# Performance work log

Hardware: AMD Instinct MI355X
Metric: run time of the kernel (lower is better)

## Reference

```python
import jax, jax.numpy as jnp
import numpy as np

B_SZ, SEQ = 2, 4096
D_MODEL, D_STATE, D_CONV, HEADDIM = 768, 128, 4, 64
D_INNER = 1536
NHEADS = D_INNER // HEADDIM  # 24
D_XBC = D_INNER + 2 * D_STATE  # 1792
D_PROJ = 2 * D_INNER + 2 * D_STATE + NHEADS  # 3352
CHUNK = 128
EPS = 1e-5


def setup_inputs():
    key = jax.random.key(0)
    ks = jax.random.split(key, 10)
    feature = jax.random.normal(ks[0], (B_SZ, SEQ, D_MODEL), jnp.float32)
    in_proj_w = jax.random.normal(ks[1], (D_PROJ, D_MODEL), jnp.float32) * 0.02
    conv_w = jax.random.normal(ks[2], (D_XBC, D_CONV), jnp.float32) * 0.2
    conv_b = jax.random.normal(ks[3], (D_XBC,), jnp.float32) * 0.02
    dt_bias = jnp.log(jnp.expm1(jax.random.uniform(ks[4], (NHEADS,), jnp.float32, 0.001, 0.1)))
    A_log = jnp.log(jax.random.uniform(ks[5], (NHEADS,), jnp.float32, 1.0, 16.0))
    D = jax.random.normal(ks[6], (NHEADS,), jnp.float32) * 0.1 + 1.0
    norm_w = jnp.ones((D_INNER,), jnp.float32)
    out_proj_w = jax.random.normal(ks[7], (D_MODEL, D_INNER), jnp.float32) * 0.02
    gate1 = jnp.float32(0.6)
    return {"feature": feature, "gate1": gate1, "in_proj_w": in_proj_w, "conv_w": conv_w,
            "conv_b": conv_b, "dt_bias": dt_bias, "A_log": A_log, "D": D,
            "norm_w": norm_w, "out_proj_w": out_proj_w}


def segsum(x):
    # x: (..., T) -> (..., T, T); out[..., i, j] = sum_{k=j+1..i} x[..., k]; -inf above diagonal
    T = x.shape[-1]
    xc = jnp.cumsum(x, axis=-1)
    d = xc[..., :, None] - xc[..., None, :]
    mask = jnp.tril(jnp.ones((T, T), bool))
    return jnp.where(mask, d, -jnp.inf)


def ssd(xd, Adt, B, C):
    # Chunked SSD (Mamba2 selective scan). xd: (b,L,H,P) = x*dt; Adt: (b,L,H); B,C: (b,L,N)
    b, L, H, P = xd.shape
    c, Q = L // CHUNK, CHUNK
    xd = xd.reshape(b, c, Q, H, P)
    Adt = Adt.reshape(b, c, Q, H).transpose(0, 3, 1, 2)          # (b,H,c,Q)
    Bc = B.reshape(b, c, Q, -1)
    Cc = C.reshape(b, c, Q, -1)
    A_cum = jnp.cumsum(Adt, axis=-1)                             # (b,H,c,Q)
    Lmat = jnp.exp(segsum(Adt))                                  # (b,H,c,Q,Q)
    CB = jnp.einsum('bcln,bcsn->bcls', Cc, Bc)                   # (b,c,Q,Q)
    Y_diag = jnp.einsum('bcls,bhcls,bcshp->bclhp', CB, Lmat, xd)
    decay_states = jnp.exp(A_cum[..., -1:] - A_cum)              # (b,H,c,Q)
    states = jnp.einsum('bcln,bhcl,bclhp->bchpn', Bc, decay_states, xd)  # (b,c,H,P,N)
    A_last = A_cum[..., -1]                                      # (b,H,c)
    decay_chunk = jnp.exp(segsum(jnp.pad(A_last, ((0, 0), (0, 0), (1, 0)))))  # (b,H,c+1,c+1)
    states_pad = jnp.concatenate([jnp.zeros_like(states[:, :1]), states], axis=1)
    prev = jnp.einsum('bhzc,bchpn->bzhpn', decay_chunk, states_pad)[:, :-1]   # state at chunk start
    Y_off = jnp.einsum('bcln,bhcl,bchpn->bclhp', Cc, jnp.exp(A_cum), prev)
    return (Y_diag + Y_off).reshape(b, L, H, P)


def reference(feature, gate1, in_proj_w, conv_w, conv_b, dt_bias, A_log, D, norm_w, out_proj_w):
    b, L, _ = feature.shape
    zxbcdt = feature @ in_proj_w.T                               # (b,L,3352)
    z = zxbcdt[..., :D_INNER]
    xBC = zxbcdt[..., D_INNER:D_INNER + D_XBC]
    dt = jax.nn.softplus(zxbcdt[..., -NHEADS:] + dt_bias)       # (b,L,H)
    # causal depthwise conv1d (kernel=4) + SiLU
    xp = jnp.pad(xBC, ((0, 0), (D_CONV - 1, 0), (0, 0)))
    xconv = sum(conv_w[:, k] * xp[:, k:k + L, :] for k in range(D_CONV)) + conv_b
    xBC = jax.nn.silu(xconv)
    x = xBC[..., :D_INNER].reshape(b, L, NHEADS, HEADDIM)
    Bm = xBC[..., D_INNER:D_INNER + D_STATE]
    Cm = xBC[..., D_INNER + D_STATE:]
    A = -jnp.exp(A_log)                                          # (H,)
    y = ssd(x * dt[..., None], dt * A, Bm, Cm) + D[:, None] * x  # skip term D*x
    y = y.reshape(b, L, D_INNER)
    # gated RMSNorm (norm_before_gate=False): gate first, then rmsnorm
    y = y * jax.nn.silu(z)
    y = y * jax.lax.rsqrt(jnp.mean(y * y, axis=-1, keepdims=True) + EPS) * norm_w
    out = y @ out_proj_w.T                                       # out_proj (bias=False)
    return jax.nn.sigmoid(gate1) * out + feature
```

## Files before the change

### kernel.cpp

```cpp
#include <hip/hip_runtime.h>
#include <hip/hip_bf16.h>
#include <math.h>

#define B_SZ 2
#define SEQ 4096
#define DMODEL 768
#define DSTATE 128
#define HEADDIM 64
#define DINNER 1536
#define NHEADS 24
#define DXBC 1792
#define DPROJ 3352
#define NPAD1 3456
#define CHUNK 128
#define NCHUNK 32
#define ROWS (B_SZ*SEQ)
#define LDTC 136
#define LDTT 132
#define LDE 136
#define LDE2 132
#define LDEY 65

typedef float floatx4 __attribute__((ext_vector_type(4)));
typedef __bf16 bf16x8 __attribute__((ext_vector_type(8)));

__device__ __forceinline__ float sigmoidf_(float x){ return 1.f/(1.f+__expf(-x)); }
__device__ __forceinline__ float siluf_(float x){ return x/(1.f+__expf(-x)); }
__device__ __forceinline__ float softplusf_(float x){ return (x>20.f)? x : __logf(1.f+__expf(x)); }
__device__ __forceinline__ __bf16 cvt_bf(float x){ __hip_bfloat16 t = __float2bfloat16(x); return *(__bf16*)&t; }

__device__ __forceinline__ void gload_lds16(const __hip_bfloat16* g, __hip_bfloat16* l){
    __builtin_amdgcn_global_load_lds(
        (const __attribute__((address_space(1))) void*)g,
        (__attribute__((address_space(3))) void*)l, 16, 0, 0);
}

__global__ __launch_bounds__(512)
void gemm1_mfma(const __hip_bfloat16* __restrict__ A,
                const __hip_bfloat16* __restrict__ W,
                __hip_bfloat16* __restrict__ z16, __hip_bfloat16* __restrict__ xbc16,
                float* __restrict__ dtb, const float* __restrict__ dt_bias)
{
    __shared__ __align__(16) char smem[49152];
    __hip_bfloat16* Asm = (__hip_bfloat16*)smem;
    __hip_bfloat16* Wsm = Asm + 256*64;
    const int tid = threadIdx.x;
    const int lane = tid & 63, wave = tid >> 6;
    const int blk = blockIdx.x;
    const int m_tile = ((blk & 7) << 2) | ((blk >> 3) & 3);
    const int bx = blk >> 5;
    const int bm = m_tile*256, bn = bx*128;
    const int wm = (wave & 3)*64, wn = (wave >> 2)*64;
    const int r16 = lane & 15, qbase = lane >> 4, sw = r16 & 7;
    floatx4 acc[4][4] = {};
    for (int k0 = 0; k0 < DMODEL; k0 += 64) {
#pragma unroll
        for (int j = 0; j < 4; ++j) {
            int cc = j*512 + tid;
            int row = cc >> 3, jc = cc & 7;
            int sj = jc ^ (row & 7);
            gload_lds16(A + (size_t)(bm+row)*DMODEL + k0 + sj*8, Asm + cc*8);
        }
#pragma unroll
        for (int j = 0; j < 2; ++j) {
            int cc = j*512 + tid;
            int row = cc >> 3, jc = cc & 7;
            int sj = jc ^ (row & 7);
            gload_lds16(W + (size_t)(bn+row)*DMODEL + k0 + sj*8, Wsm + cc*8);
        }
        __syncthreads();
#pragma unroll
        for (int ks = 0; ks < 2; ++ks) {
            const int kq = ((qbase + ks*4) ^ sw)*8;
            bf16x8 af[4], wf[4];
#pragma unroll
            for (int i = 0; i < 4; ++i) {
                af[i] = *(const bf16x8*)(Asm + (wm + i*16 + r16)*64 + kq);
                wf[i] = *(const bf16x8*)(Wsm + (wn + i*16 + r16)*64 + kq);
            }
#pragma unroll
            for (int mi = 0; mi < 4; ++mi)
#pragma unroll
                for (int ni = 0; ni < 4; ++ni)
                    acc[mi][ni] = __builtin_amdgcn_mfma_f32_16x16x32_bf16(
                        af[mi], wf[ni], acc[mi][ni], 0, 0, 0);
        }
        __syncthreads();
    }
    const int col = lane & 15, rowq = (lane >> 4)*4;
    if (bx == 26) {
        if (wn == 0) {
#pragma unroll
            for (int mi = 0; mi < 4; ++mi)
#pragma unroll
                for (int ni = 0; ni < 2; ++ni) {
                    int h = ni*16 + col;
                    if (h < NHEADS)
#pragma unroll
                        for (int r = 0; r < 4; ++r) {
                            int m = bm + wm + mi*16 + rowq + r;
                            dtb[(size_t)m*NHEADS + h] =
                                softplusf_(acc[mi][ni][r] + dt_bias[h]);
                        }
                }
        }
        return;
    }
    __hip_bfloat16* Tsm = (__hip_bfloat16*)smem;
    __hip_bfloat16* dst; int ldd;
    if (bx < 12) { dst = z16 + bn;            ldd = DINNER; }
    else         { dst = xbc16 + bn - DINNER; ldd = DXBC;  }
    for (int half = 0; half < 2; ++half) {
        if (((wave & 3) >> 1) == half) {
#pragma unroll
            for (int mi = 0; mi < 4; ++mi)
#pragma unroll
                for (int ni = 0; ni < 4; ++ni)
#pragma unroll
                    for (int r = 0; r < 4; ++r)
                        Tsm[(wm - half*128 + mi*16 + rowq + r)*LDE + wn + ni*16 + col] =
                            __float2bfloat16(acc[mi][ni][r]);
        }
        __syncthreads();
#pragma unroll
        for (int it = 0; it < 4; ++it) {
            int e = it*512 + tid;
            int row = e >> 4, c0 = (e & 15)*8;
            bf16x8 v = *(const bf16x8*)(Tsm + row*LDE + c0);
            *(bf16x8*)(dst + (size_t)(bm + half*128 + row)*ldd + c0) = v;
        }
        __syncthreads();
    }
}

__global__ __launch_bounds__(256)
void gemm2_mfma(const __hip_bfloat16* __restrict__ A,
                const __hip_bfloat16* __restrict__ W,
                float* __restrict__ C,
                const float* __restrict__ gate, const float* __restrict__ resid,
                const float* __restrict__ rowsq)
{
    __shared__ __align__(16) char smem[33792];
    __shared__ float scale_lds[128];
    __hip_bfloat16* Asm = (__hip_bfloat16*)smem;
    __hip_bfloat16* Wsm = Asm + 128*64;
    const int tid = threadIdx.x;
    const int lane = tid & 63, wave = tid >> 6;
    const int blk = blockIdx.x;
    const int mblk = blk & 63;
    const int m_tile = ((mblk & 7) << 3) | (mblk >> 3);
    const int bm = m_tile*128, bn = (blk >> 6)*128;
    const int wm = (wave & 1)*64, wn = (wave >> 1)*64;
    const int r16 = lane & 15, qbase = lane >> 4, sw = r16 & 7;
    floatx4 acc[4][4] = {};
    for (int k0 = 0; k0 < DINNER; k0 += 64) {
#pragma unroll
        for (int j = 0; j < 4; ++j) {
            int cc = j*256 + tid;
            int row = cc >> 3, jc = cc & 7;
            int sj = jc ^ (row & 7);
            gload_lds16(A + (size_t)(bm+row)*DINNER + k0 + sj*8, Asm + cc*8);
        }
#pragma unroll
        for (int j = 0; j < 4; ++j) {
            int cc = j*256 + tid;
            int row = cc >> 3, jc = cc & 7;
            int sj = jc ^ (row & 7);
            gload_lds16(W + (size_t)(bn+row)*DINNER + k0 + sj*8, Wsm + cc*8);
        }
        __syncthreads();
#pragma unroll
        for (int ks = 0; ks < 2; ++ks) {
            const int kq = ((qbase + ks*4) ^ sw)*8;
            bf16x8 af[4], wf[4];
#pragma unroll
            for (int i = 0; i < 4; ++i) {
                af[i] = *(const bf16x8*)(Asm + (wm + i*16 + r16)*64 + kq);
                wf[i] = *(const bf16x8*)(Wsm + (wn + i*16 + r16)*64 + kq);
            }
#pragma unroll
            for (int mi = 0; mi < 4; ++mi)
#pragma unroll
                for (int ni = 0; ni < 4; ++ni)
                    acc[mi][ni] = __builtin_amdgcn_mfma_f32_16x16x32_bf16(
                        af[mi], wf[ni], acc[mi][ni], 0, 0, 0);
        }
        __syncthreads();
    }
    if (tid < 128)
        scale_lds[tid] = rsqrtf(rowsq[bm + tid] * (1.f/DINNER) + 1e-5f);
    float gs = sigmoidf_(gate[0]);
    __syncthreads();
    const int col = lane & 15, rowq = (lane >> 4)*4;
    float* Tsm = (float*)smem;
    for (int half = 0; half < 2; ++half) {
        if ((wave & 1) == half) {
#pragma unroll
            for (int mi = 0; mi < 4; ++mi)
#pragma unroll
                for (int ni = 0; ni < 4; ++ni)
#pragma unroll
                    for (int r = 0; r < 4; ++r)
                        Tsm[(mi*16 + rowq + r)*LDE2 + wn + ni*16 + col] = acc[mi][ni][r];
        }
        __syncthreads();
#pragma unroll
        for (int it = 0; it < 8; ++it) {
            int e = it*256 + tid;
            int row = e >> 5, c0 = (e & 31)*4;
            float4 v = *(const float4*)(Tsm + row*LDE2 + c0);
            float sc = gs * scale_lds[half*64 + row];
            size_t off = (size_t)(bm + half*64 + row)*DMODEL + bn + c0;
            float4 rv = *(const float4*)(resid + off);
            v.x = sc*v.x + rv.x; v.y = sc*v.y + rv.y;
            v.z = sc*v.z + rv.z; v.w = sc*v.w + rv.w;
            *(float4*)(C + off) = v;
        }
        __syncthreads();
    }
}

#define NC1 (ROWS*DMODEL)
#define NC2 (NPAD1*DMODEL)
#define NC3 (DMODEL*DINNER)
#define NV1 (NC1/8)
#define NV2 (NC2/8)
#define NV3 (NC3/8)
#define NVR (ROWS/8)
__global__ __launch_bounds__(256)
void cast_all(const float* __restrict__ feature, const float* __restrict__ in_w,
              const float* __restrict__ out_w, const float* __restrict__ nw,
              __hip_bfloat16* __restrict__ fbf, __hip_bfloat16* __restrict__ wbf,
              __hip_bfloat16* __restrict__ owbf, float* __restrict__ rowsq)
{
    int v = blockIdx.x*256 + threadIdx.x;
    if (v < NV1) {
        int i = v*8;
        float4 a = *(const float4*)(feature + i);
        float4 b = *(const float4*)(feature + i + 4);
        bf16x8 o;
        o[0]=cvt_bf(a.x); o[1]=cvt_bf(a.y); o[2]=cvt_bf(a.z); o[3]=cvt_bf(a.w);
        o[4]=cvt_bf(b.x); o[5]=cvt_bf(b.y); o[6]=cvt_bf(b.z); o[7]=cvt_bf(b.w);
        *(bf16x8*)(fbf + i) = o;
    } else if (v < NV1 + NV2) {
        int j = (v - NV1)*8;
        int n = j / DMODEL, k = j - n*DMODEL;
        bf16x8 o;
        if (n < DPROJ) {
            const float* s = in_w + (size_t)n*DMODEL + k;
            float4 a = *(const float4*)(s);
            float4 b = *(const float4*)(s + 4);
            o[0]=cvt_bf(a.x); o[1]=cvt_bf(a.y); o[2]=cvt_bf(a.z); o[3]=cvt_bf(a.w);
            o[4]=cvt_bf(b.x); o[5]=cvt_bf(b.y); o[6]=cvt_bf(b.z); o[7]=cvt_bf(b.w);
        } else {
#pragma unroll
            for (int q = 0; q < 8; ++q) o[q] = (__bf16)0.f;
        }
        *(bf16x8*)(wbf + j) = o;
    } else if (v < NV1 + NV2 + NV3) {
        int j = (v - NV1 - NV2)*8;
        int k = j % DINNER;
        float4 a  = *(const float4*)(out_w + j);
        float4 b  = *(const float4*)(out_w + j + 4);
        float4 na = *(const float4*)(nw + k);
        float4 nb = *(const float4*)(nw + k + 4);
        bf16x8 o;
        o[0]=cvt_bf(a.x*na.x); o[1]=cvt_bf(a.y*na.y); o[2]=cvt_bf(a.z*na.z); o[3]=cvt_bf(a.w*na.w);
        o[4]=cvt_bf(b.x*nb.x); o[5]=cvt_bf(b.y*nb.y); o[6]=cvt_bf(b.z*nb.z); o[7]=cvt_bf(b.w*nb.w);
        *(bf16x8*)(owbf + j) = o;
    } else if (v < NV1 + NV2 + NV3 + NVR) {
        int j = (v - NV1 - NV2 - NV3)*8;
        float4 z = {0.f, 0.f, 0.f, 0.f};
        *(float4*)(rowsq + j) = z;
        *(float4*)(rowsq + j + 4) = z;
    }
}

__global__ __launch_bounds__(512)
void conv_scan_k(const __hip_bfloat16* __restrict__ xbc16, const float* __restrict__ cw,
                 const float* __restrict__ cbias,
                 __hip_bfloat16* __restrict__ x_t,
                 __hip_bfloat16* __restrict__ B_n, __hip_bfloat16* __restrict__ B_t,
                 __hip_bfloat16* __restrict__ C_n,
                 const float* __restrict__ dtb, const float* __restrict__ A_log,
                 float* __restrict__ acum)
{
    int xb = blockIdx.x;
    int tid = threadIdx.x;
    if (xb >= 14) {
        __shared__ float wtot;
        int h = xb - 14, c = blockIdx.y, b = blockIdx.z;
        int lane = tid & 63;
        float s = 0.f;
        if (tid < 128) {
            float Aa = -__expf(A_log[h]);
            s = dtb[((size_t)b*SEQ + c*CHUNK + tid)*NHEADS + h] * Aa;
#pragma unroll
            for (int off = 1; off < 64; off <<= 1) {
                float t = __shfl_up(s, off);
                if (lane >= off) s += t;
            }
            if (tid == 63) wtot = s;
        }
        __syncthreads();
        if (tid >= 64 && tid < 128) s += wtot;
        if (tid < 128)
            acum[((b*NHEADS+h)*NCHUNK + c)*CHUNK + tid] = s;
        return;
    }
    __shared__ __align__(16) __hip_bfloat16 in[131*LDTC];
    __shared__ __align__(16) __hip_bfloat16 T[128*LDTT];
    int ct = xb, lt = blockIdx.y, b = blockIdx.z;
    int base = lt*128;
    for (int it = 0; it < 2096; it += 512) {
        int e = it + tid; if (e >= 2096) break;
        int row = e >> 4, c0 = (e & 15)*8;
        int l = base - 3 + row;
        bf16x8 v;
        if (l < 0) { for (int j = 0; j < 8; ++j) v[j] = (__bf16)0.f; }
        else v = *(const bf16x8*)(xbc16 + ((size_t)b*SEQ + l)*DXBC + ct*128 + c0);
        *(bf16x8*)(in + row*LDTC + c0) = v;
    }
    __syncthreads();
    int ch = tid & 127, lh = tid >> 7, l0 = lh*32;
    int g = ct*128 + ch;
    float w0 = cw[g*4+0], w1 = cw[g*4+1], w2 = cw[g*4+2], w3 = cw[g*4+3];
    float bias = cbias[g];
    float a0 = __bfloat162float(in[(l0+0)*LDTC + ch]);
    float a1 = __bfloat162float(in[(l0+1)*LDTC + ch]);
    float a2 = __bfloat162float(in[(l0+2)*LDTC + ch]);
#pragma unroll
    for (int li = 0; li < 32; ++li) {
        float a3 = __bfloat162float(in[(l0+li+3)*LDTC + ch]);
        float o = siluf_(bias + w0*a0 + w1*a1 + w2*a2 + w3*a3);
        a0 = a1; a1 = a2; a2 = a3;
        __hip_bfloat16 ob = __float2bfloat16(o);
        size_t rr = (size_t)b*SEQ + base + l0 + li;
        if (ct == 12)      B_n[rr*DSTATE + ch] = ob;
        else if (ct == 13) C_n[rr*DSTATE + ch] = ob;
        if (ct <= 12)
            T[ch*LDTT + l0 + li] = ob;
    }
    if (ct <= 12) {
        __syncthreads();
        __hip_bfloat16* dst = (ct < 12) ? x_t : B_t;
#pragma unroll
        for (int it = 0; it < 4; ++it) {
            int e = it*512 + tid;
            int chn = e >> 4, c0 = (e & 15)*8;
            int g2 = ct*128 + chn;
            size_t trow = (ct < 12)
                ? ((size_t)b*NHEADS + (g2>>6))*HEADDIM + (g2 & 63)
                : (size_t)b*DSTATE + chn;
            bf16x8 v = *(const bf16x8*)(T + chn*LDTT + c0);
            *(bf16x8*)(dst + trow*SEQ + base + c0) = v;
        }
    }
}

__global__ __launch_bounds__(256)
void cbst_k(const __hip_bfloat16* __restrict__ B_n, const __hip_bfloat16* __restrict__ C_n,
            __hip_bfloat16* __restrict__ CB16,
            const __hip_bfloat16* __restrict__ x_t, const __hip_bfloat16* __restrict__ B_t,
            const float* __restrict__ dtb, const float* __restrict__ acum,
            __hip_bfloat16* __restrict__ states)
{
    __shared__ __align__(16) __hip_bfloat16 BT[128*128];
    __shared__ float f[128];
    int bid = blockIdx.x;
    int tid = threadIdx.x, lane = tid & 63, wave = tid >> 6;
    if (bid < 64) {
        int c = bid & 31, b = bid >> 5;
        size_t base = (size_t)b*SEQ + c*CHUNK;
        int r16 = lane & 15, kq = (lane>>4)*8;
        floatx4 acc[2][8] = {};
#pragma unroll
        for (int ks = 0; ks < 4; ++ks) {
            int k0 = ks*32 + kq;
            bf16x8 af[2], bfv[8];
#pragma unroll
            for (int mt = 0; mt < 2; ++mt)
                af[mt] = *(const bf16x8*)(C_n + (base + (wave*2+mt)*16 + r16)*DSTATE + k0);
#pragma unroll
            for (int st = 0; st < 8; ++st)
                bfv[st] = *(const bf16x8*)(B_n + (base + st*16 + r16)*DSTATE + k0);
#pragma unroll
            for (int mt = 0; mt < 2; ++mt)
#pragma unroll
                for (int st = 0; st < 8; ++st)
                    if (st <= wave*2+mt)
                        acc[mt][st] = __builtin_amdgcn_mfma_f32_16x16x32_bf16(
                            af[mt], bfv[st], acc[mt][st], 0,0,0);
        }
        size_t cbb = (size_t)(b*NCHUNK+c)*CHUNK*CHUNK;
        int scol = lane & 15, rowq = (lane>>4)*4;
#pragma unroll
        for (int mt = 0; mt < 2; ++mt)
#pragma unroll
            for (int st = 0; st < 8; ++st)
                if (st <= wave*2+mt)
#pragma unroll
                    for (int r = 0; r < 4; ++r)
                        CB16[cbb + (size_t)((wave*2+mt)*16 + rowq + r)*CHUNK + st*16 + scol] =
                            __float2bfloat16(acc[mt][st][r]);
        return;
    }
    int t = bid - 64;
    int c = t & 31;
    int h = (t>>5) % NHEADS;
    int b = t/(32*NHEADS);
    int arow = ((b*NHEADS+h)*NCHUNK + c)*CHUNK;
    size_t rbase = (size_t)b*SEQ + c*CHUNK;
    int cl = c*CHUNK;
#pragma unroll
    for (int j = 0; j < 8; ++j) {
        int cc = j*256 + tid;
        int n = cc >> 4, chk = cc & 15;
        int sj = chk ^ (n & 7);
        gload_lds16(B_t + ((size_t)b*DSTATE + n)*SEQ + cl + sj*8, BT + cc*8);
    }
    if (tid < 128) {
        float alast = acum[arow + 127];
        f[tid] = dtb[(rbase + tid)*NHEADS + h] * __expf(alast - acum[arow + tid]);
    }
    __syncthreads();
    int r16 = lane & 15, kq = (lane>>4)*8;
    size_t xtb = ((size_t)b*NHEADS + h)*HEADDIM;
    floatx4 acc[8] = {};
#pragma unroll
    for (int ks = 0; ks < 4; ++ks) {
        int k0 = ks*32 + kq;
        bf16x8 xa = *(const bf16x8*)(x_t + (xtb + wave*16 + r16)*SEQ + cl + k0);
        bf16x8 af;
#pragma unroll
        for (int j = 0; j < 8; ++j)
            af[j] = (__bf16)((float)xa[j] * f[k0 + j]);
        int chL = k0 >> 3;
        bf16x8 bfv[8];
#pragma unroll
        for (int nt = 0; nt < 8; ++nt) {
            int row = nt*16 + r16;
            bfv[nt] = *(const bf16x8*)(BT + (row*16 + (chL ^ (row & 7)))*8);
        }
#pragma unroll
        for (int nt = 0; nt < 8; ++nt)
            acc[nt] = __builtin_amdgcn_mfma_f32_16x16x32_bf16(af, bfv[nt], acc[nt], 0,0,0);
    }
    size_t sb = ((size_t)(b*NCHUNK+c)*NHEADS + h)*(HEADDIM*DSTATE);
    int ncol = lane & 15, rowq = (lane>>4)*4;
#pragma unroll
    for (int nt = 0; nt < 8; ++nt)
#pragma unroll
        for (int r = 0; r < 4; ++r)
            states[sb + (size_t)(wave*16 + rowq + r)*DSTATE + nt*16 + ncol] =
                __float2bfloat16(acc[nt][r]);
}

__global__ __launch_bounds__(64)
void recur_k(__hip_bfloat16* __restrict__ states, const float* __restrict__ acum)
{
    int pb = blockIdx.x & 15;
    int bh = blockIdx.x >> 4;
    int h = bh % NHEADS, b = bh / NHEADS;
    int voff = (pb*64 + threadIdx.x)*8;
    const size_t cstride = (size_t)NHEADS*HEADDIM*DSTATE;
    size_t base0 = ((size_t)(b*NCHUNK)*NHEADS + h)*(HEADDIM*DSTATE) + voff;
    bf16x8 st[NCHUNK];
    float ev[NCHUNK];
#pragma unroll
    for (int c = 0; c < NCHUNK; ++c)
        st[c] = *(const bf16x8*)(states + base0 + (size_t)c*cstride);
#pragma unroll
    for (int c = 0; c < NCHUNK; ++c)
        ev[c] = __expf(acum[((b*NHEADS+h)*NCHUNK + c)*CHUNK + 127]);
    float S[8] = {};
#pragma unroll
    for (int c = 0; c < NCHUNK; ++c) {
        bf16x8 pv;
#pragma unroll
        for (int j = 0; j < 8; ++j) {
            pv[j] = (__bf16)S[j];
            S[j] = S[j]*ev[c] + (float)st[c][j];
        }
        *(bf16x8*)(states + base0 + (size_t)c*cstride) = pv;
    }
}

__global__ __launch_bounds__(512, 4)
void y_mfma(const __hip_bfloat16* __restrict__ x_t, const __hip_bfloat16* __restrict__ z16,
            const __hip_bfloat16* __restrict__ C_n, const __hip_bfloat16* __restrict__ CB16,
            const __hip_bfloat16* __restrict__ states, const float* __restrict__ dtb,
            const float* __restrict__ acum, const float* __restrict__ Dp,
            __hip_bfloat16* __restrict__ y16, float* __restrict__ rowsq)
{
    __shared__ __align__(16) char smem[32768];
    __hip_bfloat16* XT = (__hip_bfloat16*)smem;
    __hip_bfloat16* ST = XT + 64*128;
    __shared__ __align__(16) float Tsm[128*LDEY];
    __shared__ float ac[128], dts[128], gk[128];
    const int tid = threadIdx.x, lane = tid & 63, wave = tid >> 6;
    const int r16 = lane & 15, kq = (lane>>4)*8;
    const int l = wave*16 + r16;
    const int pcol = lane & 15, rowq = (lane>>4)*4;
    const int erow = tid >> 2, ec0 = (tid & 3)*16;
    const int NU = B_SZ*NHEADS*NCHUNK;
    {
        int u = blockIdx.x;
        int c = u & 31, h = (u>>5) % NHEADS, b = u/(32*NHEADS);
        size_t xtb = ((size_t)b*NHEADS + h)*HEADDIM;
        size_t sb  = ((size_t)(b*NCHUNK+c)*NHEADS + h)*(HEADDIM*DSTATE);
        int cl = c*CHUNK;
#pragma unroll
        for (int j = 0; j < 2; ++j) {
            int cc = j*512 + tid;
            int p = cc >> 4, ch = cc & 15;
            int sj = ch ^ (p & 7);
            gload_lds16(x_t + (xtb + p)*SEQ + cl + sj*8, XT + cc*8);
            gload_lds16(states + sb + (size_t)p*DSTATE + sj*8, ST + cc*8);
        }
    }
#pragma unroll 1
    for (int u = blockIdx.x; u < NU; u += 512) {
        int c = u & 31;
        int h = (u>>5) % NHEADS;
        int b = u/(32*NHEADS);
        int arow = ((b*NHEADS+h)*NCHUNK + c)*CHUNK;
        size_t rbase = (size_t)b*SEQ + c*CHUNK;
        size_t cbb = (size_t)(b*NCHUNK+c)*CHUNK*CHUNK;
        if (tid < 128) {
            ac[tid]  = acum[arow + tid];
            dts[tid] = dtb[(rbase + tid)*NHEADS + h];
        }
        __syncthreads();
        if (tid < 128)
            gk[tid] = __expf(ac[tid & 96] - ac[tid]) * dts[tid];
        bf16x8 cb[4], cv[4];
#pragma unroll
        for (int ks = 0; ks < 4; ++ks) {
            cb[ks] = *(const bf16x8*)(CB16 + cbb + (size_t)l*CHUNK + ks*32 + kq);
            cv[ks] = *(const bf16x8*)(C_n + (rbase + l)*DSTATE + ks*32 + kq);
        }
        bf16x8 zA = *(const bf16x8*)(z16 + (rbase + erow)*DINNER + h*HEADDIM + ec0);
        bf16x8 zB = *(const bf16x8*)(z16 + (rbase + erow)*DINNER + h*HEADDIM + ec0 + 8);
        __syncthreads();
        float acl = ac[l];
        float Dh = Dp[h];
        floatx4 acc[4] = {};
        int nks = (wave >> 1) + 1;
#pragma unroll
        for (int ks = 0; ks < 4; ++ks) {
            if (ks < nks) {
                int k0 = ks*32 + kq;
                float fl = __expf(acl - ac[ks*32]);
                bf16x8 af;
#pragma unroll
                for (int j = 0; j < 8; ++j) {
                    int s = k0 + j;
                    float w = (s <= l) ? (float)cb[ks][j] * (fl * gk[s]) : 0.f;
                    if (s == l) w += Dh;
                    af[j] = (__bf16)w;
                }
                int chL = k0 >> 3;
                bf16x8 bfv[4];
#pragma unroll
                for (int pt = 0; pt < 4; ++pt) {
                    int row = pt*16 + r16;
                    bfv[pt] = *(const bf16x8*)(XT + (row*16 + (chL ^ (row & 7)))*8);
                }
#pragma unroll
                for (int pt = 0; pt < 4; ++pt)
                    acc[pt] = __builtin_amdgcn_mfma_f32_16x16x32_bf16(af, bfv[pt], acc[pt], 0,0,0);
            }
        }
        float eal = __expf(acl);
#pragma unroll
        for (int ks = 0; ks < 4; ++ks) {
            int k0 = ks*32 + kq;
            bf16x8 af;
#pragma unroll
            for (int j = 0; j < 8; ++j)
                af[j] = (__bf16)((float)cv[ks][j] * eal);
            int chL = k0 >> 3;
            bf16x8 bfv[4];
#pragma unroll
            for (int pt = 0; pt < 4; ++pt) {
                int row = pt*16 + r16;
                bfv[pt] = *(const bf16x8*)(ST + (row*16 + (chL ^ (row & 7)))*8);
            }
#pragma unroll
            for (int pt = 0; pt < 4; ++pt)
                acc[pt] = __builtin_amdgcn_mfma_f32_16x16x32_bf16(af, bfv[pt], acc[pt], 0,0,0);
        }
        __syncthreads();
        int un = u + 512;
        if (un < NU) {
            int c2 = un & 31, h2 = (un>>5) % NHEADS, b2 = un/(32*NHEADS);
            size_t xtb2 = ((size_t)b2*NHEADS + h2)*HEADDIM;
            size_t sb2  = ((size_t)(b2*NCHUNK+c2)*NHEADS + h2)*(HEADDIM*DSTATE);
            int cl2 = c2*CHUNK;
#pragma unroll
            for (int j = 0; j < 2; ++j) {
                int cc = j*512 + tid;
                int p = cc >> 4, ch = cc & 15;
                int sj = ch ^ (p & 7);
                gload_lds16(x_t + (xtb2 + p)*SEQ + cl2 + sj*8, XT + cc*8);
                gload_lds16(states + sb2 + (size_t)p*DSTATE + sj*8, ST + cc*8);
            }
        }
#pragma unroll
        for (int pt = 0; pt < 4; ++pt)
#pragma unroll
            for (int r = 0; r < 4; ++r)
                Tsm[(wave*16 + rowq + r)*LDEY + pt*16 + pcol] = acc[pt][r];
        __syncthreads();
        {
            float s = 0.f; bf16x8 o1, o2;
#pragma unroll
            for (int j2 = 0; j2 < 8; ++j2) {
                float g = Tsm[erow*LDEY + ec0 + j2] * siluf_(__bfloat162float(zA[j2]));
                o1[j2] = cvt_bf(g); s += g*g;
            }
#pragma unroll
            for (int j2 = 0; j2 < 8; ++j2) {
                float g = Tsm[erow*LDEY + ec0 + 8 + j2] * siluf_(__bfloat162float(zB[j2]));
                o2[j2] = cvt_bf(g); s += g*g;
            }
            size_t grow = rbase + erow;
            *(bf16x8*)(y16 + grow*DINNER + h*HEADDIM + ec0)     = o1;
            *(bf16x8*)(y16 + grow*DINNER + h*HEADDIM + ec0 + 8) = o2;
            s += __shfl_xor(s, 1); s += __shfl_xor(s, 2);
            if ((tid & 3) == 0)
                atomicAdd(rowsq + grow, s);
        }
    }
}

extern "C" void kernel_launch(void* const* d_in, const int* in_sizes, int n_in,
                              void* d_out, int out_size, void* d_ws, size_t ws_size,
                              hipStream_t stream)
{
    const float* feature = (const float*)d_in[0];
    const float* gate1   = (const float*)d_in[1];
    const float* in_w    = (const float*)d_in[2];
    const float* conv_w  = (const float*)d_in[3];
    const float* conv_b  = (const float*)d_in[4];
    const float* dt_bias = (const float*)d_in[5];
    const float* A_log   = (const float*)d_in[6];
    const float* Dp      = (const float*)d_in[7];
    const float* norm_w  = (const float*)d_in[8];
    const float* out_w   = (const float*)d_in[9];
    float* out = (float*)d_out;

    char* p = (char*)d_ws;
    __hip_bfloat16* z16   = (__hip_bfloat16*)p; p += (size_t)ROWS*DINNER*2;
    __hip_bfloat16* xbc16 = (__hip_bfloat16*)p; p += (size_t)ROWS*DXBC*2;
    __hip_bfloat16* x_t   = (__hip_bfloat16*)p; p += (size_t)ROWS*DINNER*2;
    __hip_bfloat16* B_n   = (__hip_bfloat16*)p; p += (size_t)ROWS*DSTATE*2;
    __hip_bfloat16* B_t   = (__hip_bfloat16*)p; p += (size_t)ROWS*DSTATE*2;
    __hip_bfloat16* C_n   = (__hip_bfloat16*)p; p += (size_t)ROWS*DSTATE*2;
    float* dtb    = (float*)p;            p += (size_t)ROWS*NHEADS*4;
    float* acum   = (float*)p;            p += (size_t)B_SZ*NHEADS*NCHUNK*CHUNK*4;
    float* rowsq  = (float*)p;            p += (size_t)ROWS*4;
    __hip_bfloat16* CB16 = (__hip_bfloat16*)p; p += (size_t)B_SZ*NCHUNK*CHUNK*CHUNK*2;
    __hip_bfloat16* states = (__hip_bfloat16*)p; p += (size_t)B_SZ*NCHUNK*NHEADS*HEADDIM*DSTATE*2;
    __hip_bfloat16* y16  = (__hip_bfloat16*)p; p += (size_t)ROWS*DINNER*2;
    __hip_bfloat16* fbf  = (__hip_bfloat16*)p; p += (size_t)ROWS*DMODEL*2;
    __hip_bfloat16* wbf  = (__hip_bfloat16*)p; p += (size_t)NPAD1*DMODEL*2;
    __hip_bfloat16* owbf = (__hip_bfloat16*)p; p += (size_t)DMODEL*DINNER*2;

    cast_all<<<(NV1+NV2+NV3+NVR+255)/256, 256, 0, stream>>>(feature, in_w, out_w, norm_w,
                                                            fbf, wbf, owbf, rowsq);

    gemm1_mfma<<<27*32, 512, 0, stream>>>(fbf, wbf, z16, xbc16, dtb, dt_bias);
    conv_scan_k<<<dim3(14 + NHEADS, 32, B_SZ), 512, 0, stream>>>(
        xbc16, conv_w, conv_b, x_t, B_n, B_t, C_n, dtb, A_log, acum);
    cbst_k<<<64 + B_SZ*NHEADS*NCHUNK, 256, 0, stream>>>(
        B_n, C_n, CB16, x_t, B_t, dtb, acum, states);
    recur_k<<<B_SZ*NHEADS*16, 64, 0, stream>>>(states, acum);
    y_mfma<<<512, 512, 0, stream>>>(x_t, z16, C_n, CB16, states,
                                    dtb, acum, Dp, y16, rowsq);
    gemm2_mfma<<<6*64, 256, 0, stream>>>(y16, owbf, out, gate1, feature, rowsq);
}
```

Baseline: 264.1 us.

## Double-buffer gemm2 LDS, pack scan heads per block, stage B in LDS for CB

The out-projection GEMM now double-buffers its A and W tiles in LDS, issuing the next tile's loads before computing the current one, with one barrier per k-step instead of two. This is meant to hide global load latency, at the cost of doubling LDS to 64KB, which may reduce occupancy. The cumsum blocks in conv_scan now handle four heads each with all 512 threads active, so far fewer mostly-idle blocks are launched. In cbst_k, the CB blocks load the B chunk once into swizzled LDS rather than re-reading it from global memory in every wave.

```diff
diff --git a/kernel.cpp b/kernel.cpp
--- a/kernel.cpp
+++ b/kernel.cpp
@@ -140,10 +140,12 @@
                 const float* __restrict__ gate, const float* __restrict__ resid,
                 const float* __restrict__ rowsq)
 {
-    __shared__ __align__(16) char smem[33792];
+    __shared__ __align__(16) char smem[65536];
     __shared__ float scale_lds[128];
-    __hip_bfloat16* Asm = (__hip_bfloat16*)smem;
-    __hip_bfloat16* Wsm = Asm + 128*64;
+    __hip_bfloat16* A0 = (__hip_bfloat16*)smem;
+    __hip_bfloat16* W0 = A0 + 128*64;
+    __hip_bfloat16* A1 = W0 + 128*64;
+    __hip_bfloat16* W1 = A1 + 128*64;
     const int tid = threadIdx.x;
     const int lane = tid & 63, wave = tid >> 6;
     const int blk = blockIdx.x;
@@ -153,40 +155,47 @@
     const int wm = (wave & 1)*64, wn = (wave >> 1)*64;
     const int r16 = lane & 15, qbase = lane >> 4, sw = r16 & 7;
     floatx4 acc[4][4] = {};
-    for (int k0 = 0; k0 < DINNER; k0 += 64) {
-#pragma unroll
-        for (int j = 0; j < 4; ++j) {
-            int cc = j*256 + tid;
-            int row = cc >> 3, jc = cc & 7;
-            int sj = jc ^ (row & 7);
-            gload_lds16(A + (size_t)(bm+row)*DINNER + k0 + sj*8, Asm + cc*8);
-        }
-#pragma unroll
-        for (int j = 0; j < 4; ++j) {
-            int cc = j*256 + tid;
-            int row = cc >> 3, jc = cc & 7;
-            int sj = jc ^ (row & 7);
-            gload_lds16(W + (size_t)(bn+row)*DINNER + k0 + sj*8, Wsm + cc*8);
-        }
-        __syncthreads();
-#pragma unroll
-        for (int ks = 0; ks < 2; ++ks) {
-            const int kq = ((qbase + ks*4) ^ sw)*8;
-            bf16x8 af[4], wf[4];
-#pragma unroll
-            for (int i = 0; i < 4; ++i) {
-                af[i] = *(const bf16x8*)(Asm + (wm + i*16 + r16)*64 + kq);
-                wf[i] = *(const bf16x8*)(Wsm + (wn + i*16 + r16)*64 + kq);
-            }
-#pragma unroll
-            for (int mi = 0; mi < 4; ++mi)
-#pragma unroll
-                for (int ni = 0; ni < 4; ++ni)
-                    acc[mi][ni] = __builtin_amdgcn_mfma_f32_16x16x32_bf16(
-                        af[mi], wf[ni], acc[mi][ni], 0, 0, 0);
-        }
-        __syncthreads();
-    }
+#define G2_STAGE(SA, SW, K0) { \
+    _Pragma("unroll") \
+    for (int j = 0; j < 4; ++j) { \
+        int cc = j*256 + tid; \
+        int row = cc >> 3, jc = cc & 7; \
+        int sj = jc ^ (row & 7); \
+        gload_lds16(A + (size_t)(bm+row)*DINNER + (K0) + sj*8, (SA) + cc*8); \
+    } \
+    _Pragma("unroll") \
+    for (int j = 0; j < 4; ++j) { \
+        int cc = j*256 + tid; \
+        int row = cc >> 3, jc = cc & 7; \
+        int sj = jc ^ (row & 7); \
+        gload_lds16(W + (size_t)(bn+row)*DINNER + (K0) + sj*8, (SW) + cc*8); \
+    } }
+#define G2_COMPUTE(CA, CW) { \
+    _Pragma("unroll") \
+    for (int ks = 0; ks < 2; ++ks) { \
+        const int kq = ((qbase + ks*4) ^ sw)*8; \
+        bf16x8 af[4], wf[4]; \
+        _Pragma("unroll") \
+        for (int i = 0; i < 4; ++i) { \
+            af[i] = *(const bf16x8*)((CA) + (wm + i*16 + r16)*64 + kq); \
+            wf[i] = *(const bf16x8*)((CW) + (wn + i*16 + r16)*64 + kq); \
+        } \
+        _Pragma("unroll") \
+        for (int mi = 0; mi < 4; ++mi) \
+            _Pragma("unroll") \
+            for (int ni = 0; ni < 4; ++ni) \
+                acc[mi][ni] = __builtin_amdgcn_mfma_f32_16x16x32_bf16( \
+                    af[mi], wf[ni], acc[mi][ni], 0, 0, 0); \
+    } }
+    G2_STAGE(A0, W0, 0);
+    __syncthreads();
+#pragma unroll 1
+    for (int t = 0; t < 23; ++t) {
+        if (t & 1) { G2_STAGE(A0, W0, (t+1)*64); G2_COMPUTE(A1, W1); }
+        else       { G2_STAGE(A1, W1, (t+1)*64); G2_COMPUTE(A0, W0); }
+        __syncthreads();
+    }
+    G2_COMPUTE(A1, W1);
     if (tid < 128)
         scale_lds[tid] = rsqrtf(rowsq[bm + tid] * (1.f/DINNER) + 1e-5f);
     float gs = sigmoidf_(gate[0]);
@@ -288,24 +297,22 @@
     int xb = blockIdx.x;
     int tid = threadIdx.x;
     if (xb >= 14) {
-        __shared__ float wtot;
-        int h = xb - 14, c = blockIdx.y, b = blockIdx.z;
-        int lane = tid & 63;
-        float s = 0.f;
-        if (tid < 128) {
-            float Aa = -__expf(A_log[h]);
-            s = dtb[((size_t)b*SEQ + c*CHUNK + tid)*NHEADS + h] * Aa;
-#pragma unroll
-            for (int off = 1; off < 64; off <<= 1) {
-                float t = __shfl_up(s, off);
-                if (lane >= off) s += t;
-            }
-            if (tid == 63) wtot = s;
-        }
-        __syncthreads();
-        if (tid >= 64 && tid < 128) s += wtot;
-        if (tid < 128)
-            acum[((b*NHEADS+h)*NCHUNK + c)*CHUNK + tid] = s;
+        __shared__ float wtot[4];
+        int c = blockIdx.y, b = blockIdx.z;
+        int g2 = tid >> 7;
+        int h = (xb - 14)*4 + g2;
+        int l = tid & 127, lane = tid & 63;
+        float Aa = -__expf(A_log[h]);
+        float s = dtb[((size_t)b*SEQ + c*CHUNK + l)*NHEADS + h] * Aa;
+#pragma unroll
+        for (int off = 1; off < 64; off <<= 1) {
+            float t = __shfl_up(s, off);
+            if (lane >= off) s += t;
+        }
+        if ((tid & 127) == 63) wtot[g2] = s;
+        __syncthreads();
+        if ((tid & 127) >= 64) s += wtot[g2];
+        acum[((b*NHEADS+h)*NCHUNK + c)*CHUNK + l] = s;
         return;
     }
     __shared__ __align__(16) __hip_bfloat16 in[131*LDTC];
@@ -372,18 +379,29 @@
     if (bid < 64) {
         int c = bid & 31, b = bid >> 5;
         size_t base = (size_t)b*SEQ + c*CHUNK;
+#pragma unroll
+        for (int j = 0; j < 8; ++j) {
+            int cc = j*256 + tid;
+            int n = cc >> 4, chk = cc & 15;
+            int sj = chk ^ (n & 7);
+            gload_lds16(B_n + (base + n)*DSTATE + sj*8, BT + cc*8);
+        }
+        __syncthreads();
         int r16 = lane & 15, kq = (lane>>4)*8;
         floatx4 acc[2][8] = {};
 #pragma unroll
         for (int ks = 0; ks < 4; ++ks) {
             int k0 = ks*32 + kq;
+            int chL = k0 >> 3;
             bf16x8 af[2], bfv[8];
 #pragma unroll
             for (int mt = 0; mt < 2; ++mt)
                 af[mt] = *(const bf16x8*)(C_n + (base + (wave*2+mt)*16 + r16)*DSTATE + k0);
 #pragma unroll
-            for (int st = 0; st < 8; ++st)
-                bfv[st] = *(const bf16x8*)(B_n + (base + st*16 + r16)*DSTATE + k0);
+            for (int st = 0; st < 8; ++st) {
+                int row = st*16 + r16;
+                bfv[st] = *(const bf16x8*)(BT + (row*16 + (chL ^ (row & 7)))*8);
+            }
 #pragma unroll
             for (int mt = 0; mt < 2; ++mt)
 #pragma unroll
@@ -672,7 +690,7 @@
                                                             fbf, wbf, owbf, rowsq);
 
     gemm1_mfma<<<27*32, 512, 0, stream>>>(fbf, wbf, z16, xbc16, dtb, dt_bias);
-    conv_scan_k<<<dim3(14 + NHEADS, 32, B_SZ), 512, 0, stream>>>(
+    conv_scan_k<<<dim3(14 + NHEADS/4, 32, B_SZ), 512, 0, stream>>>(
         xbc16, conv_w, conv_b, x_t, B_n, B_t, C_n, dtb, A_log, acum);
     cbst_k<<<64 + B_SZ*NHEADS*NCHUNK, 256, 0, stream>>>(
         B_n, C_n, CB16, x_t, B_t, dtb, acum, states);
```

Result: slower. 288.7 us (+9.3%).
